# Kernel optimization log

Hardware: AMD Instinct MI355X
Metric: run time of the kernel (lower is better)

## Reference

```python
import jax, jax.numpy as jnp
import numpy as np

B, S, D, E2 = 64, 512, 1024, 1024  # batch, enc seq len, dec hidden, 2*enc hidden


def setup_inputs() -> dict:
    key = jax.random.key(0)
    ks = jax.random.split(key, 5)
    scale = 1.0 / np.sqrt(D + E2)
    return {
        "dec_state": jax.random.normal(ks[0], (B, D), jnp.float32),
        "enc_states": jax.random.normal(ks[1], (B, S, E2), jnp.float32),
        "att_mask": jnp.ones((B, S), jnp.int32),
        "w_weight": jax.random.normal(ks[2], (D, D + E2), jnp.float32) * scale,
        "w_bias": jax.random.normal(ks[3], (D,), jnp.float32) * scale,
        "v_weight": jax.random.normal(ks[4], (D,), jnp.float32) * (1.0 / np.sqrt(D)),
    }


def reference(dec_state, enc_states, att_mask, w_weight, w_bias, v_weight):
    # Additive (Bahdanau) attention. Split the concat-linear into two GEMMs:
    # tanh(W [dec; enc] + b) == tanh(dec @ Wd^T + enc @ We^T + b) -- same math,
    # avoids materializing the repeated/concatenated [B,S,D+2E] tensor.
    Wd = w_weight[:, :dec_state.shape[-1]]          # [D, D]
    We = w_weight[:, dec_state.shape[-1]:]          # [D, 2E]
    dec_proj = jnp.einsum('bd,kd->bk', dec_state, Wd)        # [B, D]
    enc_proj = jnp.einsum('bse,ke->bsk', enc_states, We)     # [B, S, D]
    energy = jnp.tanh(enc_proj + dec_proj[:, None, :] + w_bias)  # [B, S, D]
    attention = jnp.einsum('bsk,k->bs', energy, v_weight)    # [B, S]
    attention = jnp.where(att_mask == 0, -jnp.inf, attention)
    att_weights = jax.nn.softmax(attention, axis=1)          # [B, S]
    att_out = jnp.einsum('bs,bse->be', att_weights, enc_states)[:, None, :]  # [B,1,2E]
    return att_out
```

## Files before the change

kernel.cpp:

```cpp
#include <hip/hip_runtime.h>
#include <hip/hip_bf16.h>
#include <math.h>

#define B_  64
#define S_  512
#define D_  1024
#define E2_ 1024
#define WROW (D_ + E2_)
#define NTILES 4

typedef __attribute__((ext_vector_type(8))) short bf16x8;
typedef __attribute__((ext_vector_type(4))) float f32x4;
typedef __attribute__((ext_vector_type(8))) unsigned short u16x8;

__device__ __forceinline__ unsigned short f2bf(float f) {
    unsigned u = __float_as_uint(f);
    u = (u + 0x7FFFu + ((u >> 16) & 1u)) >> 16;
    return (unsigned short)u;
}

__device__ __forceinline__ void load_lds16(const void* g, void* l) {
    __builtin_amdgcn_global_load_lds(
        (__attribute__((address_space(1))) void*)(void*)g,
        (__attribute__((address_space(3))) void*)l,
        16, 0, 0);
}

__device__ __forceinline__ float fast_tanh(float x) {
    float ax = fminf(fabsf(x), 16.0f);
    float t  = __builtin_amdgcn_exp2f(ax * 2.8853900817779268f);
    float r  = (t - 1.0f) * __builtin_amdgcn_rcpf(t + 1.0f);
    return copysignf(r, x);
}

__global__ __launch_bounds__(256) void prep_kernel(
        const float* __restrict__ w,
        const float* __restrict__ dec,
        const float* __restrict__ bias,
        unsigned short* __restrict__ web,
        float* __restrict__ t)
{
    const int blk = blockIdx.x;
    const int tid = threadIdx.x;

    if (blk < D_) {
        const int k = blk;
        const int j = tid * 4;
        float4 a = *reinterpret_cast<const float4*>(w + (size_t)k * WROW + D_ + j);
        ushort4 o;
        o.x = f2bf(a.x); o.y = f2bf(a.y); o.z = f2bf(a.z); o.w = f2bf(a.w);
        *reinterpret_cast<ushort4*>(web + (size_t)k * E2_ + j) = o;
    } else {
        __shared__ float wrow[D_];
        __shared__ float red[256];
        const int k = blk - D_;
        const float* wr = w + (size_t)k * WROW;
        for (int i = tid; i < D_; i += 256) wrow[i] = wr[i];
        __syncthreads();

        const int b = tid >> 2;
        const int q = tid & 3;
        const float* dp = dec + b * D_ + q * 256;
        const float* wp = wrow + q * 256;
        float acc = 0.f;
        #pragma unroll 8
        for (int i = 0; i < 256; ++i) acc = fmaf(dp[i], wp[i], acc);
        red[tid] = acc;
        __syncthreads();
        if (q == 0) {
            float s = red[tid] + red[tid + 1] + red[tid + 2] + red[tid + 3];
            t[b * D_ + k] = s + bias[k];
        }
    }
}

#define BME 256
#define BNE 256
#define BKE 64
#define KT_ (E2_ / BKE)

__global__ __launch_bounds__(512) void energy_mfma_kernel(
        const float* __restrict__ encf,
        const unsigned short* __restrict__ web,
        const float* __restrict__ t,
        const float* __restrict__ v,
        float* __restrict__ att_part)
{
    __shared__ __align__(16) unsigned short As[2][BME * BKE];
    __shared__ __align__(16) unsigned short Bs[2][BNE * BKE];
    __shared__ float tv_s[BNE];
    __shared__ float vv_s[BNE];
    __shared__ float red[4][BME];

    const int g     = blockIdx.x;
    const int mblk  = (g & 7) + 8 * (g >> 5);
    const int ntile = (g >> 3) & 3;

    const int m0 = mblk * BME;
    const int n0 = ntile * BNE;
    const int b  = m0 >> 9;
    const int tid = threadIdx.x;
    const int w   = tid >> 6;
    const int l   = tid & 63;
    const int wm  = w >> 2;
    const int wn  = w & 3;

    if (tid < BNE) {
        tv_s[tid] = t[b * D_ + n0 + tid];
        vv_s[tid] = v[n0 + tid];
    }

    const int arow0 = tid >> 4;
    const int acolb = (tid & 15) * 8;
    const int aswz  = (arow0 & 7) << 4;
    const float* gAf = encf + (size_t)m0 * E2_;

    const int lr8 = l >> 3;
    const int lk  = 8 * ((l & 7) ^ lr8);
    const unsigned short* gB = web + (size_t)n0 * E2_;

    const int rA = wm * 128 + (l & 15);
    const int rB = wn * 64 + (l & 15);
    const int kswz = (l & 7) << 4;
    const int khi  = (l >> 4) << 4;

    f32x4 acc[8][4] = {};
    float4 av[8];

    auto issueA = [&](int kt) {
        const int k0 = kt * BKE;
        #pragma unroll
        for (int i = 0; i < 8; ++i) {
            const int row = i * 32 + arow0;
            av[i] = *reinterpret_cast<const float4*>(
                gAf + (size_t)row * E2_ + k0 + (tid & 15) * 4);
        }
    };
    auto writeA = [&](int bf) {
        #pragma unroll
        for (int i = 0; i < 8; ++i) {
            const int row = i * 32 + arow0;
            unsigned p0, p1;
            asm("v_cvt_pk_bf16_f32 %0, %1, %2"
                : "=v"(p0) : "v"(av[i].x), "v"(av[i].y));
            asm("v_cvt_pk_bf16_f32 %0, %1, %2"
                : "=v"(p1) : "v"(av[i].z), "v"(av[i].w));
            uint2 o; o.x = p0; o.y = p1;
            *reinterpret_cast<uint2*>(
                (char*)As[bf] + row * 128 + (acolb ^ aswz)) = o;
        }
    };
    auto issueB = [&](int bf, int kt) {
        const int k0 = kt * BKE;
        #pragma unroll
        for (int r = 0; r < 4; ++r) {
            const int c = r * 8 + w;
            const int row = c * 8 + lr8;
            load_lds16(gB + (size_t)row * E2_ + k0 + lk,
                       (char*)Bs[bf] + c * 1024);
        }
    };

    issueA(0);
    issueB(0, 0);
    writeA(0);
    issueA(1);
    asm volatile("s_waitcnt vmcnt(8) lgkmcnt(0)" ::: "memory");
    __builtin_amdgcn_s_barrier();
    __builtin_amdgcn_sched_barrier(0);

    for (int kt = 0; kt < KT_; ++kt) {
        const int cur = kt & 1;
        const int nxt = cur ^ 1;

        if (kt + 1 < KT_) issueB(nxt, kt + 1);
        __builtin_amdgcn_sched_barrier(0);

        {
            const int kb = khi ^ kswz;
            bf16x8 a[8], bb[4];
            #pragma unroll
            for (int mi = 0; mi < 8; ++mi)
                a[mi] = *reinterpret_cast<const bf16x8*>(
                    (const char*)As[cur] + (rA + mi * 16) * 128 + kb);
            #pragma unroll
            for (int ni = 0; ni < 4; ++ni)
                bb[ni] = *reinterpret_cast<const bf16x8*>(
                    (const char*)Bs[cur] + (rB + ni * 16) * 128 + kb);
            __builtin_amdgcn_s_setprio(1);
            #pragma unroll
            for (int mi = 0; mi < 8; ++mi)
                #pragma unroll
                for (int ni = 0; ni < 4; ++ni)
                    acc[mi][ni] = __builtin_amdgcn_mfma_f32_16x16x32_bf16(
                        a[mi], bb[ni], acc[mi][ni], 0, 0, 0);
            __builtin_amdgcn_s_setprio(0);
        }
        __builtin_amdgcn_sched_barrier(0);

        if (kt + 1 < KT_) writeA(nxt);
        if (kt + 2 < KT_) issueA(kt + 2);
        __builtin_amdgcn_sched_barrier(0);

        {
            const int kb = (64 + khi) ^ kswz;
            bf16x8 a[8], bb[4];
            #pragma unroll
            for (int mi = 0; mi < 8; ++mi)
                a[mi] = *reinterpret_cast<const bf16x8*>(
                    (const char*)As[cur] + (rA + mi * 16) * 128 + kb);
            #pragma unroll
            for (int ni = 0; ni < 4; ++ni)
                bb[ni] = *reinterpret_cast<const bf16x8*>(
                    (const char*)Bs[cur] + (rB + ni * 16) * 128 + kb);
            __builtin_amdgcn_s_setprio(1);
            #pragma unroll
            for (int mi = 0; mi < 8; ++mi)
                #pragma unroll
                for (int ni = 0; ni < 4; ++ni)
                    acc[mi][ni] = __builtin_amdgcn_mfma_f32_16x16x32_bf16(
                        a[mi], bb[ni], acc[mi][ni], 0, 0, 0);
            __builtin_amdgcn_s_setprio(0);
        }
        __builtin_amdgcn_sched_barrier(0);

        if (kt + 2 < KT_) {
            asm volatile("s_waitcnt vmcnt(8) lgkmcnt(0)" ::: "memory");
        } else if (kt + 1 < KT_) {
            asm volatile("s_waitcnt vmcnt(0) lgkmcnt(0)" ::: "memory");
        }
        __builtin_amdgcn_s_barrier();
        __builtin_amdgcn_sched_barrier(0);
    }

    #pragma unroll
    for (int mi = 0; mi < 8; ++mi) {
        float P[4] = {0.f, 0.f, 0.f, 0.f};
        #pragma unroll
        for (int ni = 0; ni < 4; ++ni) {
            const int nl = wn * 64 + ni * 16 + (l & 15);
            const float tvv = tv_s[nl];
            const float vvv = vv_s[nl];
            #pragma unroll
            for (int j = 0; j < 4; ++j) {
                float e = fast_tanh(acc[mi][ni][j] + tvv);
                P[j] = fmaf(e, vvv, P[j]);
            }
        }
        #pragma unroll
        for (int j = 0; j < 4; ++j) {
            float p = P[j];
            p += __shfl_xor(p, 1);
            p += __shfl_xor(p, 2);
            p += __shfl_xor(p, 4);
            p += __shfl_xor(p, 8);
            if ((l & 15) == 0)
                red[wn][wm * 128 + mi * 16 + (l >> 4) * 4 + j] = p;
        }
    }
    __syncthreads();
    if (tid < BME)
        att_part[(size_t)(m0 + tid) * NTILES + ntile] =
            (red[0][tid] + red[1][tid]) + (red[2][tid] + red[3][tid]);
}

__global__ __launch_bounds__(256) void attout_sm_kernel(
        const float* __restrict__ att_part,
        const int* __restrict__ mask,
        const float* __restrict__ enc,
        float* __restrict__ out_part)
{
    __shared__ float wall[S_];
    __shared__ float red[256];
    const int b  = blockIdx.y;
    const int sc = blockIdx.x;
    const int tid = threadIdx.x;

    float x[2];
    bool mv[2];
    #pragma unroll
    for (int j = 0; j < 2; ++j) {
        const int s = tid + j * 256;
        float4 p = *reinterpret_cast<const float4*>(
            att_part + (size_t)(b * S_ + s) * NTILES);
        x[j] = (p.x + p.y) + (p.z + p.w);
        mv[j] = (mask[b * S_ + s] != 0);
        if (!mv[j]) x[j] = -INFINITY;
    }
    float m = fmaxf(x[0], x[1]);
    red[tid] = m;
    __syncthreads();
    for (int o = 128; o > 0; o >>= 1) {
        if (tid < o) red[tid] = fmaxf(red[tid], red[tid + o]);
        __syncthreads();
    }
    m = red[0];
    __syncthreads();
    float e0 = mv[0] ? expf(x[0] - m) : 0.f;
    float e1 = mv[1] ? expf(x[1] - m) : 0.f;
    red[tid] = e0 + e1;
    __syncthreads();
    for (int o = 128; o > 0; o >>= 1) {
        if (tid < o) red[tid] += red[tid + o];
        __syncthreads();
    }
    const float inv = 1.f / red[0];
    wall[tid] = e0 * inv;
    wall[tid + 256] = e1 * inv;
    __syncthreads();

    const float* wsm = wall + sc * 64;
    const float4* ep = reinterpret_cast<const float4*>(
        enc + ((size_t)b * S_ + sc * 64) * E2_) + tid;
    float4 acc = {0.f, 0.f, 0.f, 0.f};
    #pragma unroll 8
    for (int s = 0; s < 64; ++s) {
        float4 e4 = ep[(size_t)s * (E2_ / 4)];
        const float ws = wsm[s];
        acc.x = fmaf(ws, e4.x, acc.x);
        acc.y = fmaf(ws, e4.y, acc.y);
        acc.z = fmaf(ws, e4.z, acc.z);
        acc.w = fmaf(ws, e4.w, acc.w);
    }
    reinterpret_cast<float4*>(out_part + ((size_t)sc * B_ + b) * E2_)[tid] = acc;
}

__global__ __launch_bounds__(256) void attout_reduce_kernel(
        const float* __restrict__ out_part,
        float* __restrict__ out)
{
    const int idx = blockIdx.x * 256 + threadIdx.x;
    const int n4 = (B_ * E2_) / 4;
    const float4* p = reinterpret_cast<const float4*>(out_part);
    float4 r = p[idx];
    #pragma unroll
    for (int c = 1; c < 8; ++c) {
        float4 q = p[idx + c * n4];
        r.x += q.x; r.y += q.y; r.z += q.z; r.w += q.w;
    }
    reinterpret_cast<float4*>(out)[idx] = r;
}

extern "C" void kernel_launch(void* const* d_in, const int* in_sizes, int n_in,
                              void* d_out, int out_size, void* d_ws, size_t ws_size,
                              hipStream_t stream) {
    const float* dec  = (const float*)d_in[0];
    const float* enc  = (const float*)d_in[1];
    const int*   mask = (const int*)d_in[2];
    const float* w    = (const float*)d_in[3];
    const float* bias = (const float*)d_in[4];
    const float* v    = (const float*)d_in[5];
    float* out = (float*)d_out;

    float* t_buf    = (float*)d_ws;
    float* att_part = t_buf + B_ * D_;
    float* out_part = att_part + B_ * S_ * NTILES;
    unsigned short* web = (unsigned short*)(out_part + 8 * B_ * E2_);

    prep_kernel<<<2 * D_, 256, 0, stream>>>(w, dec, bias, web, t_buf);
    energy_mfma_kernel<<<512, 512, 0, stream>>>(enc, web, t_buf, v, att_part);
    attout_sm_kernel<<<dim3(8, B_), 256, 0, stream>>>(att_part, mask,
                                                      enc, out_part);
    attout_reduce_kernel<<<(B_ * E2_ / 4) / 256, 256, 0, stream>>>(out_part, out);
}
```

Before: 137.3 us.

## Load B operand directly from global into registers, bypassing LDS

The pre-converted bf16 weight tile is now read straight from global memory into register fragments per wave instead of staged through LDS via global_load_lds. The B fragments are double-buffered in registers across a 2x-unrolled k loop, and the explicit vmcnt waits are dropped in favour of compiler-inserted waits. This removes the B LDS buffers and LDS read traffic, cutting LDS footprint and bank pressure. In exchange it adds VGPR pressure (16 extra bf16x8 registers), makes global loads less coalesced, duplicates weight reads across waves sharing the same wn, and loses the explicit prefetch-depth control.

```diff
diff --git a/kernel.cpp b/kernel.cpp
--- a/kernel.cpp
+++ b/kernel.cpp
@@ -11,19 +11,11 @@
 
 typedef __attribute__((ext_vector_type(8))) short bf16x8;
 typedef __attribute__((ext_vector_type(4))) float f32x4;
-typedef __attribute__((ext_vector_type(8))) unsigned short u16x8;
 
 __device__ __forceinline__ unsigned short f2bf(float f) {
     unsigned u = __float_as_uint(f);
     u = (u + 0x7FFFu + ((u >> 16) & 1u)) >> 16;
     return (unsigned short)u;
-}
-
-__device__ __forceinline__ void load_lds16(const void* g, void* l) {
-    __builtin_amdgcn_global_load_lds(
-        (__attribute__((address_space(1))) void*)(void*)g,
-        (__attribute__((address_space(3))) void*)l,
-        16, 0, 0);
 }
 
 __device__ __forceinline__ float fast_tanh(float x) {
@@ -87,7 +79,6 @@
         float* __restrict__ att_part)
 {
     __shared__ __align__(16) unsigned short As[2][BME * BKE];
-    __shared__ __align__(16) unsigned short Bs[2][BNE * BKE];
     __shared__ float tv_s[BNE];
     __shared__ float vv_s[BNE];
     __shared__ float red[4][BME];
@@ -115,17 +106,16 @@
     const int aswz  = (arow0 & 7) << 4;
     const float* gAf = encf + (size_t)m0 * E2_;
 
-    const int lr8 = l >> 3;
-    const int lk  = 8 * ((l & 7) ^ lr8);
-    const unsigned short* gB = web + (size_t)n0 * E2_;
-
     const int rA = wm * 128 + (l & 15);
-    const int rB = wn * 64 + (l & 15);
     const int kswz = (l & 7) << 4;
     const int khi  = (l >> 4) << 4;
 
+    const unsigned short* gBf =
+        web + (size_t)(n0 + wn * 64 + (l & 15)) * E2_ + (l >> 4) * 8;
+
     f32x4 acc[8][4] = {};
     float4 av[8];
+    bf16x8 bbA[8], bbB[8];
 
     auto issueA = [&](int kt) {
         const int k0 = kt * BKE;
@@ -150,87 +140,61 @@
                 (char*)As[bf] + row * 128 + (acolb ^ aswz)) = o;
         }
     };
-    auto issueB = [&](int bf, int kt) {
-        const int k0 = kt * BKE;
-        #pragma unroll
-        for (int r = 0; r < 4; ++r) {
-            const int c = r * 8 + w;
-            const int row = c * 8 + lr8;
-            load_lds16(gB + (size_t)row * E2_ + k0 + lk,
-                       (char*)Bs[bf] + c * 1024);
-        }
-    };
+
+    #define LOADB4(dst, kt, kk)                                              \
+        { _Pragma("unroll")                                                  \
+          for (int ni = 0; ni < 4; ++ni)                                     \
+              dst[(kk) * 4 + ni] = *reinterpret_cast<const bf16x8*>(         \
+                  gBf + (size_t)(ni * 16) * E2_ + (kt) * BKE + (kk) * 32); }
+
+    #define MFMA_HALF(cur, bb, kk)                                           \
+        {   const int kb = ((kk) * 64 + khi) ^ kswz;                         \
+            bf16x8 a[8];                                                     \
+            _Pragma("unroll")                                                \
+            for (int mi = 0; mi < 8; ++mi)                                   \
+                a[mi] = *reinterpret_cast<const bf16x8*>(                    \
+                    (const char*)As[cur] + (rA + mi * 16) * 128 + kb);       \
+            __builtin_amdgcn_s_setprio(1);                                   \
+            _Pragma("unroll")                                                \
+            for (int mi = 0; mi < 8; ++mi)                                   \
+                _Pragma("unroll")                                            \
+                for (int ni = 0; ni < 4; ++ni)                               \
+                    acc[mi][ni] = __builtin_amdgcn_mfma_f32_16x16x32_bf16(   \
+                        a[mi], bb[(kk) * 4 + ni], acc[mi][ni], 0, 0, 0);     \
+            __builtin_amdgcn_s_setprio(0);                                   \
+        }
+
+    #define KT_BODY(kt, cur, bbU, bbF)                                       \
+        {   const int nxt = (cur) ^ 1;                                       \
+            if ((kt) + 1 < KT_) LOADB4(bbF, (kt) + 1, 0);                    \
+            __builtin_amdgcn_sched_barrier(0);                               \
+            MFMA_HALF(cur, bbU, 0);                                          \
+            __builtin_amdgcn_sched_barrier(0);                               \
+            if ((kt) + 1 < KT_) writeA(nxt);                                 \
+            if ((kt) + 2 < KT_) issueA((kt) + 2);                            \
+            if ((kt) + 1 < KT_) LOADB4(bbF, (kt) + 1, 1);                    \
+            __builtin_amdgcn_sched_barrier(0);                               \
+            MFMA_HALF(cur, bbU, 1);                                          \
+            __builtin_amdgcn_sched_barrier(0);                               \
+            asm volatile("s_waitcnt lgkmcnt(0)" ::: "memory");               \
+            __builtin_amdgcn_s_barrier();                                    \
+            __builtin_amdgcn_sched_barrier(0);                               \
+        }
 
     issueA(0);
-    issueB(0, 0);
+    LOADB4(bbA, 0, 0);
+    LOADB4(bbA, 0, 1);
     writeA(0);
     issueA(1);
-    asm volatile("s_waitcnt vmcnt(8) lgkmcnt(0)" ::: "memory");
+    asm volatile("s_waitcnt lgkmcnt(0)" ::: "memory");
     __builtin_amdgcn_s_barrier();
     __builtin_amdgcn_sched_barrier(0);
 
-    for (int kt = 0; kt < KT_; ++kt) {
-        const int cur = kt & 1;
-        const int nxt = cur ^ 1;
-
-        if (kt + 1 < KT_) issueB(nxt, kt + 1);
-        __builtin_amdgcn_sched_barrier(0);
-
-        {
-            const int kb = khi ^ kswz;
-            bf16x8 a[8], bb[4];
-            #pragma unroll
-            for (int mi = 0; mi < 8; ++mi)
-                a[mi] = *reinterpret_cast<const bf16x8*>(
-                    (const char*)As[cur] + (rA + mi * 16) * 128 + kb);
-            #pragma unroll
-            for (int ni = 0; ni < 4; ++ni)
-                bb[ni] = *reinterpret_cast<const bf16x8*>(
-                    (const char*)Bs[cur] + (rB + ni * 16) * 128 + kb);
-            __builtin_amdgcn_s_setprio(1);
-            #pragma unroll
-            for (int mi = 0; mi < 8; ++mi)
-                #pragma unroll
-                for (int ni = 0; ni < 4; ++ni)
-                    acc[mi][ni] = __builtin_amdgcn_mfma_f32_16x16x32_bf16(
-                        a[mi], bb[ni], acc[mi][ni], 0, 0, 0);
-            __builtin_amdgcn_s_setprio(0);
-        }
-        __builtin_amdgcn_sched_barrier(0);
-
-        if (kt + 1 < KT_) writeA(nxt);
-        if (kt + 2 < KT_) issueA(kt + 2);
-        __builtin_amdgcn_sched_barrier(0);
-
-        {
-            const int kb = (64 + khi) ^ kswz;
-            bf16x8 a[8], bb[4];
-            #pragma unroll
-            for (int mi = 0; mi < 8; ++mi)
-                a[mi] = *reinterpret_cast<const bf16x8*>(
-                    (const char*)As[cur] + (rA + mi * 16) * 128 + kb);
-            #pragma unroll
-            for (int ni = 0; ni < 4; ++ni)
-                bb[ni] = *reinterpret_cast<const bf16x8*>(
-                    (const char*)Bs[cur] + (rB + ni * 16) * 128 + kb);
-            __builtin_amdgcn_s_setprio(1);
-            #pragma unroll
-            for (int mi = 0; mi < 8; ++mi)
-                #pragma unroll
-                for (int ni = 0; ni < 4; ++ni)
-                    acc[mi][ni] = __builtin_amdgcn_mfma_f32_16x16x32_bf16(
-                        a[mi], bb[ni], acc[mi][ni], 0, 0, 0);
-            __builtin_amdgcn_s_setprio(0);
-        }
-        __builtin_amdgcn_sched_barrier(0);
-
-        if (kt + 2 < KT_) {
-            asm volatile("s_waitcnt vmcnt(8) lgkmcnt(0)" ::: "memory");
-        } else if (kt + 1 < KT_) {
-            asm volatile("s_waitcnt vmcnt(0) lgkmcnt(0)" ::: "memory");
-        }
-        __builtin_amdgcn_s_barrier();
-        __builtin_amdgcn_sched_barrier(0);
+    #pragma unroll 1
+    for (int kt2 = 0; kt2 < KT_ / 2; ++kt2) {
+        const int kt0 = kt2 * 2;
+        KT_BODY(kt0,     0, bbA, bbB);
+        KT_BODY(kt0 + 1, 1, bbB, bbA);
     }
 
     #pragma unroll
```

Result: slower. 341.8 us (+149.0%).
